# Kernel tuning notes

Hardware: AMD Instinct MI355X
Metric: run time of the kernel (lower is better)

## Reference

```python
import jax, jax.numpy as jnp
import numpy as np

N_NODES = 20000
N_EDGES = 256000
DIM = 128
N_LAYERS = 4


def _bn(x, gamma, beta, eps=1e-5):
    # BatchNorm1d in training mode: batch statistics over the node/edge axis
    mu = x.mean(0)
    var = ((x - mu) ** 2).mean(0)
    return gamma * (x - mu) * jax.lax.rsqrt(var + eps) + beta


def setup_inputs() -> dict:
    key = jax.random.key(0)
    ks = jax.random.split(key, 32)
    s = 1.0 / np.sqrt(DIM)
    inp = {
        'h': jax.random.normal(ks[0], (N_NODES, DIM), jnp.float32),
        'e': jax.random.normal(ks[1], (N_EDGES, DIM), jnp.float32),
        'src': jax.random.randint(ks[2], (N_EDGES,), 0, N_NODES, jnp.int32),
        'dst': jax.random.randint(ks[3], (N_EDGES,), 0, N_NODES, jnp.int32),
        'W_emb_h': jax.random.normal(ks[4], (DIM, DIM), jnp.float32) * s,
        'b_emb_h': jnp.zeros((DIM,), jnp.float32),
        'W_emb_e': jax.random.normal(ks[5], (DIM, DIM), jnp.float32) * s,
        'b_emb_e': jnp.zeros((DIM,), jnp.float32),
    }
    for i, nm in enumerate(['A', 'B', 'C', 'D', 'E']):
        inp[nm + 'w'] = jax.random.normal(ks[6 + i], (N_LAYERS, DIM, DIM), jnp.float32) * s
        inp[nm + 'b'] = jnp.zeros((N_LAYERS, DIM), jnp.float32)
    inp['gh'] = jnp.ones((N_LAYERS, DIM), jnp.float32)
    inp['bh'] = jnp.zeros((N_LAYERS, DIM), jnp.float32)
    inp['ge'] = jnp.ones((N_LAYERS, DIM), jnp.float32)
    inp['be'] = jnp.zeros((N_LAYERS, DIM), jnp.float32)
    return inp


def reference(h, e, src, dst, W_emb_h, b_emb_h, W_emb_e, b_emb_e,
              Aw, Ab, Bw, Bb, Cw, Cb, Dw, Db, Ew, Eb, gh, bh, ge, be):
    n_nodes = h.shape[0]
    # input embeddings
    h = h @ W_emb_h + b_emb_h
    e = e @ W_emb_e + b_emb_e
    for l in range(Aw.shape[0]):
        h_in, e_in = h, e
        Ah = h @ Aw[l] + Ab[l]
        Bh = h @ Bw[l] + Bb[l]
        Dh = h @ Dw[l] + Db[l]
        Eh = h @ Ew[l] + Eb[l]
        Ce = e @ Cw[l] + Cb[l]
        # edge gates: e_ij = D h_i + E h_j + C e_ij  (edge i->j)
        e_new = Dh[src] + Eh[dst] + Ce            # [E, D]
        sigma = jax.nn.sigmoid(e_new)
        num = jax.ops.segment_sum(sigma * Bh[src], dst, num_segments=n_nodes)
        den = jax.ops.segment_sum(sigma, dst, num_segments=n_nodes)
        h_new = Ah + num / (den + 1e-6)
        h_new = _bn(h_new, gh[l], bh[l])
        e_new = _bn(e_new, ge[l], be[l])
        # relu + residual (dropout = 0)
        h = h_in + jax.nn.relu(h_new)
        e = e_in + jax.nn.relu(e_new)
    return h
```

## Files before the change

### kernel.cpp

```cpp
#include <hip/hip_runtime.h>
#include <hip/hip_bf16.h>

typedef __attribute__((ext_vector_type(8))) short short8;
typedef __attribute__((ext_vector_type(4))) float floatx4;
typedef __attribute__((ext_vector_type(4))) unsigned short ushortx4;

__device__ __forceinline__ float bf2f(unsigned short u) {
    union { float f; unsigned int i; } v; v.i = ((unsigned int)u) << 16; return v.f;
}
__device__ __forceinline__ unsigned short f2bf(float f) {
    union { float f; unsigned int i; } v; v.f = f;
    unsigned int r = v.i + 0x7fffu + ((v.i >> 16) & 1u);
    return (unsigned short)(r >> 16);
}

__global__ void deg_count(const int* __restrict__ dst, int* __restrict__ deg, int E) {
    int i = blockIdx.x * 256 + threadIdx.x;
    if (i < E) atomicAdd(&deg[dst[i]], 1);
}

__global__ __launch_bounds__(1024) void scan_rowptr(const int* __restrict__ deg,
                                                    int* __restrict__ rowptr,
                                                    int* __restrict__ cursor, int N) {
    const int CH = 20;
    __shared__ int buf[1024];
    int t = threadIdx.x;
    int base = t * CH;
    int local[CH];
    int tot = 0;
#pragma unroll
    for (int k = 0; k < CH; ++k) {
        int i = base + k;
        int v = (i < N) ? deg[i] : 0;
        local[k] = tot;
        tot += v;
    }
    buf[t] = tot;
    __syncthreads();
    for (int off = 1; off < 1024; off <<= 1) {
        int x = (t >= off) ? buf[t - off] : 0;
        __syncthreads();
        buf[t] += x;
        __syncthreads();
    }
    int excl = buf[t] - tot;
#pragma unroll
    for (int k = 0; k < CH; ++k) {
        int i = base + k;
        if (i < N) { rowptr[i] = excl + local[k]; cursor[i] = excl + local[k]; }
    }
    if (t == 1023) rowptr[N] = buf[1023];
}

__global__ void scatter_edges(const int* __restrict__ src, const int* __restrict__ dst,
                              int* __restrict__ cursor, int* __restrict__ eix,
                              int* __restrict__ sx, int E) {
    int i = blockIdx.x * 256 + threadIdx.x;
    if (i >= E) return;
    int d = dst[i];
    int pos = atomicAdd(&cursor[d], 1);
    eix[pos] = i;
    sx[pos] = src[i];
}

__global__ void transpose_w(const float* __restrict__ Wh,
                            const float* __restrict__ We,
                            const float* __restrict__ Aw,
                            const float* __restrict__ Bw,
                            const float* __restrict__ Cw,
                            const float* __restrict__ Dw,
                            const float* __restrict__ Ew,
                            unsigned short* __restrict__ Wt) {
    int i = blockIdx.x * 256 + threadIdx.x;
    const int total = 22 * 16384;
    if (i >= total) return;
    int slot = i >> 14;
    int r = i & 16383;
    int n = r >> 7;
    int k = r & 127;
    const float* srcp;
    if (slot == 0) srcp = Wh;
    else if (slot == 1) srcp = We;
    else {
        int t = slot - 2;
        int l = t / 5, w = t % 5;
        const float* bases[5] = {Aw, Bw, Cw, Dw, Ew};
        srcp = bases[w] + l * 16384;
    }
    Wt[i] = f2bf(srcp[k * 128 + n]);
}

template <int IN_BF16, int OUT_BF16, int GATHER>
__global__ __launch_bounds__(256) void gemm128(const void* __restrict__ Ain,
                                               const int* __restrict__ ridx,
                                               const unsigned short* __restrict__ Wt,
                                               const float* __restrict__ bias,
                                               void* __restrict__ Cout, int nStrips) {
    const int lane = threadIdx.x & 63;
    const int wv = threadIdx.x >> 6;
    const int m16 = lane & 15;
    const int kg = lane >> 4;

    short8 b[4][8];
#pragma unroll
    for (int ks = 0; ks < 4; ++ks)
#pragma unroll
        for (int nt = 0; nt < 8; ++nt)
            b[ks][nt] = *(const short8*)(Wt + (nt * 16 + m16) * 128 + ks * 32 + kg * 8);

    float bv[8];
#pragma unroll
    for (int nt = 0; nt < 8; ++nt) bv[nt] = bias[nt * 16 + m16];

    const float* Af = (const float*)Ain;
    const unsigned short* Ab16 = (const unsigned short*)Ain;

    int wave = blockIdx.x * 4 + wv;
    int nw = gridDim.x * 4;
    for (int s = wave; s < nStrips; s += nw) {
        int rowA = s * 16 + m16;
        if (GATHER) rowA = ridx[rowA];
        size_t rowBase = (size_t)rowA * 128;
        short8 a[4];
#pragma unroll
        for (int ks = 0; ks < 4; ++ks) {
            int off = ks * 32 + kg * 8;
            if (IN_BF16) {
                a[ks] = *(const short8*)(Ab16 + rowBase + off);
            } else {
                floatx4 f0 = *(const floatx4*)(Af + rowBase + off);
                floatx4 f1 = *(const floatx4*)(Af + rowBase + off + 4);
                short8 t;
                t[0] = (short)f2bf(f0[0]); t[1] = (short)f2bf(f0[1]);
                t[2] = (short)f2bf(f0[2]); t[3] = (short)f2bf(f0[3]);
                t[4] = (short)f2bf(f1[0]); t[5] = (short)f2bf(f1[1]);
                t[6] = (short)f2bf(f1[2]); t[7] = (short)f2bf(f1[3]);
                a[ks] = t;
            }
        }
        floatx4 acc[8];
#pragma unroll
        for (int nt = 0; nt < 8; ++nt) acc[nt] = (floatx4){0.f, 0.f, 0.f, 0.f};
#pragma unroll
        for (int ks = 0; ks < 4; ++ks)
#pragma unroll
            for (int nt = 0; nt < 8; ++nt)
                acc[nt] = __builtin_amdgcn_mfma_f32_16x16x32_bf16(a[ks], b[ks][nt], acc[nt], 0, 0, 0);
#pragma unroll
        for (int nt = 0; nt < 8; ++nt) {
#pragma unroll
            for (int i = 0; i < 4; ++i) {
                size_t r = (size_t)s * 16 + kg * 4 + i;
                int cix = nt * 16 + m16;
                float v = acc[nt][i] + bv[nt];
                if (OUT_BF16)
                    ((unsigned short*)Cout)[r * 128 + cix] = f2bf(v);
                else
                    ((float*)Cout)[r * 128 + cix] = v;
            }
        }
    }
}

__global__ __launch_bounds__(256) void gemm_h4(const float* __restrict__ h_cur,
                                               const unsigned short* __restrict__ WtL,
                                               const float* __restrict__ Abi,
                                               const float* __restrict__ Bbi,
                                               const float* __restrict__ Dbi,
                                               const float* __restrict__ Ebi,
                                               float* __restrict__ AhB,
                                               unsigned short* __restrict__ BD16,
                                               unsigned short* __restrict__ Eh16,
                                               int nStrips) {
    const int lane = threadIdx.x & 63;
    const int wv = threadIdx.x >> 6;
    const int m16 = lane & 15;
    const int kg = lane >> 4;
    int s = blockIdx.x;
    if (s >= nStrips) return;

    const int slotmap[4] = {0, 1, 3, 4};
    const unsigned short* Wm = WtL + slotmap[wv] * 16384;
    const float* biasp = (wv == 0) ? Abi : (wv == 1) ? Bbi : (wv == 2) ? Dbi : Ebi;

    short8 b[4][8];
#pragma unroll
    for (int ks = 0; ks < 4; ++ks)
#pragma unroll
        for (int nt = 0; nt < 8; ++nt)
            b[ks][nt] = *(const short8*)(Wm + (nt * 16 + m16) * 128 + ks * 32 + kg * 8);
    float bv[8];
#pragma unroll
    for (int nt = 0; nt < 8; ++nt) bv[nt] = biasp[nt * 16 + m16];

    size_t rowBase = ((size_t)s * 16 + m16) * 128;
    short8 a[4];
#pragma unroll
    for (int ks = 0; ks < 4; ++ks) {
        int off = ks * 32 + kg * 8;
        floatx4 f0 = *(const floatx4*)(h_cur + rowBase + off);
        floatx4 f1 = *(const floatx4*)(h_cur + rowBase + off + 4);
        short8 t;
        t[0] = (short)f2bf(f0[0]); t[1] = (short)f2bf(f0[1]);
        t[2] = (short)f2bf(f0[2]); t[3] = (short)f2bf(f0[3]);
        t[4] = (short)f2bf(f1[0]); t[5] = (short)f2bf(f1[1]);
        t[6] = (short)f2bf(f1[2]); t[7] = (short)f2bf(f1[3]);
        a[ks] = t;
    }
    floatx4 acc[8];
#pragma unroll
    for (int nt = 0; nt < 8; ++nt) acc[nt] = (floatx4){0.f, 0.f, 0.f, 0.f};
#pragma unroll
    for (int ks = 0; ks < 4; ++ks)
#pragma unroll
        for (int nt = 0; nt < 8; ++nt)
            acc[nt] = __builtin_amdgcn_mfma_f32_16x16x32_bf16(a[ks], b[ks][nt], acc[nt], 0, 0, 0);

#pragma unroll
    for (int nt = 0; nt < 8; ++nt)
#pragma unroll
        for (int i = 0; i < 4; ++i) {
            size_t r = (size_t)s * 16 + kg * 4 + i;
            int c = nt * 16 + m16;
            float v = acc[nt][i] + bv[nt];
            if (wv == 0) AhB[r * 128 + c] = v;
            else if (wv == 1) BD16[r * 256 + 2 * c] = f2bf(v);
            else if (wv == 2) BD16[r * 256 + 2 * c + 1] = f2bf(v);
            else Eh16[r * 128 + c] = f2bf(v);
        }
}

template <int DO_E>
__global__ __launch_bounds__(256) void node_aggregate(unsigned short* __restrict__ Ce,
                                                      const unsigned short* __restrict__ BD16,
                                                      const unsigned short* __restrict__ Eh16,
                                                      const int* __restrict__ rowptr,
                                                      const int* __restrict__ sx,
                                                      const float* __restrict__ Ah,
                                                      float* __restrict__ h_new,
                                                      float* __restrict__ sums, int N) {
    const int q = threadIdx.x & 31;
    const int g = threadIdx.x >> 5;
    float hs[4] = {0.f, 0.f, 0.f, 0.f};
    float hq[4] = {0.f, 0.f, 0.f, 0.f};
    float es[4] = {0.f, 0.f, 0.f, 0.f};
    float eq[4] = {0.f, 0.f, 0.f, 0.f};
    for (int d = blockIdx.x * 8 + g; d < N; d += gridDim.x * 8) {
        int beg = rowptr[d], end = rowptr[d + 1];
        ushortx4 eh4 = *(const ushortx4*)(Eh16 + (size_t)d * 128 + q * 4);
        float ehf[4];
#pragma unroll
        for (int k = 0; k < 4; ++k) ehf[k] = bf2f(eh4[k]);
        float num[4] = {0.f, 0.f, 0.f, 0.f};
        float den[4] = {0.f, 0.f, 0.f, 0.f};
        int j = beg;
        for (; j + 1 < end; j += 2) {
            int s0 = sx[j], s1 = sx[j + 1];
            ushortx4 c0 = *(const ushortx4*)(Ce + (size_t)j * 128 + q * 4);
            ushortx4 c1 = *(const ushortx4*)(Ce + (size_t)(j + 1) * 128 + q * 4);
            short8 bd0 = *(const short8*)(BD16 + (size_t)s0 * 256 + q * 8);
            short8 bd1 = *(const short8*)(BD16 + (size_t)s1 * 256 + q * 8);
            ushortx4 o0, o1;
#pragma unroll
            for (int k = 0; k < 4; ++k) {
                float en0 = bf2f(c0[k]) + bf2f((unsigned short)bd0[2 * k + 1]) + ehf[k];
                float en1 = bf2f(c1[k]) + bf2f((unsigned short)bd1[2 * k + 1]) + ehf[k];
                if (DO_E) {
                    es[k] += en0 + en1;
                    eq[k] += en0 * en0 + en1 * en1;
                    o0[k] = f2bf(en0);
                    o1[k] = f2bf(en1);
                }
                float sg0 = 1.f / (1.f + __expf(-en0));
                float sg1 = 1.f / (1.f + __expf(-en1));
                den[k] += sg0 + sg1;
                num[k] += sg0 * bf2f((unsigned short)bd0[2 * k])
                        + sg1 * bf2f((unsigned short)bd1[2 * k]);
            }
            if (DO_E) {
                *(ushortx4*)(Ce + (size_t)j * 128 + q * 4) = o0;
                *(ushortx4*)(Ce + (size_t)(j + 1) * 128 + q * 4) = o1;
            }
        }
        if (j < end) {
            int s0 = sx[j];
            ushortx4 c0 = *(const ushortx4*)(Ce + (size_t)j * 128 + q * 4);
            short8 bd0 = *(const short8*)(BD16 + (size_t)s0 * 256 + q * 8);
            ushortx4 o0;
#pragma unroll
            for (int k = 0; k < 4; ++k) {
                float en0 = bf2f(c0[k]) + bf2f((unsigned short)bd0[2 * k + 1]) + ehf[k];
                if (DO_E) {
                    es[k] += en0;
                    eq[k] += en0 * en0;
                    o0[k] = f2bf(en0);
                }
                float sg0 = 1.f / (1.f + __expf(-en0));
                den[k] += sg0;
                num[k] += sg0 * bf2f((unsigned short)bd0[2 * k]);
            }
            if (DO_E) *(ushortx4*)(Ce + (size_t)j * 128 + q * 4) = o0;
        }
        floatx4 ah = *(const floatx4*)(Ah + (size_t)d * 128 + q * 4);
        floatx4 out;
#pragma unroll
        for (int k = 0; k < 4; ++k) {
            float v = ah[k] + num[k] / (den[k] + 1e-6f);
            out[k] = v;
            hs[k] += v;
            hq[k] += v * v;
        }
        *(floatx4*)(h_new + (size_t)d * 128 + q * 4) = out;
    }
    __shared__ float ls[512];
    ls[threadIdx.x] = 0.f;
    ls[256 + threadIdx.x] = 0.f;
    __syncthreads();
#pragma unroll
    for (int k = 0; k < 4; ++k) {
        atomicAdd(&ls[q * 4 + k], hs[k]);
        atomicAdd(&ls[128 + q * 4 + k], hq[k]);
        if (DO_E) {
            atomicAdd(&ls[256 + q * 4 + k], es[k]);
            atomicAdd(&ls[384 + q * 4 + k], eq[k]);
        }
    }
    __syncthreads();
    atomicAdd(&sums[threadIdx.x], ls[threadIdx.x]);
    if (DO_E) atomicAdd(&sums[256 + threadIdx.x], ls[256 + threadIdx.x]);
}

__global__ void finalize_stats(const float* __restrict__ sums,
                               const float* __restrict__ gh,
                               const float* __restrict__ bh,
                               const float* __restrict__ ge,
                               const float* __restrict__ be,
                               float* __restrict__ coef, int N, int E) {
    int c = threadIdx.x;
    if (c >= 128) return;
    float muh = sums[c] / (float)N;
    float vh = fmaxf(sums[128 + c] / (float)N - muh * muh, 0.f);
    float rsh = rsqrtf(vh + 1e-5f);
    float g = gh[c], bt = bh[c];
    coef[c] = g * rsh;
    coef[128 + c] = bt - g * rsh * muh;
    float mue = sums[256 + c] / (float)E;
    float ve = fmaxf(sums[384 + c] / (float)E - mue * mue, 0.f);
    float rse = rsqrtf(ve + 1e-5f);
    float g2 = ge[c], b2 = be[c];
    coef[256 + c] = g2 * rse;
    coef[384 + c] = b2 - g2 * rse * mue;
}

__global__ __launch_bounds__(256) void h_update(const float* __restrict__ h_new,
                                                const float* __restrict__ coef,
                                                float* __restrict__ h_cur,
                                                float* __restrict__ out, int N) {
    const int c = threadIdx.x & 127;
    float sa = coef[c], sb = coef[128 + c];
    int total = N * 128;
    for (int i = blockIdx.x * blockDim.x + threadIdx.x; i < total; i += gridDim.x * blockDim.x) {
        float v = h_new[i] * sa + sb;
        v = v > 0.f ? v : 0.f;
        float h = h_cur[i] + v;
        h_cur[i] = h;
        if (out) out[i] = h;
    }
}

__global__ __launch_bounds__(256) void e_update(const unsigned short* __restrict__ e_new,
                                                const float* __restrict__ coef,
                                                unsigned short* __restrict__ e_cur, int E) {
    int total8 = E * 16;
    for (int idx = blockIdx.x * blockDim.x + threadIdx.x; idx < total8;
         idx += gridDim.x * blockDim.x) {
        int c8 = (idx & 15) * 8;
        short8 en = *(const short8*)(e_new + (size_t)idx * 8);
        short8 ec = *(const short8*)(e_cur + (size_t)idx * 8);
        floatx4 sa0 = *(const floatx4*)(coef + 256 + c8);
        floatx4 sa1 = *(const floatx4*)(coef + 256 + c8 + 4);
        floatx4 sb0 = *(const floatx4*)(coef + 384 + c8);
        floatx4 sb1 = *(const floatx4*)(coef + 384 + c8 + 4);
        short8 r;
#pragma unroll
        for (int k = 0; k < 8; ++k) {
            float sa = (k < 4) ? sa0[k] : sa1[k - 4];
            float sb = (k < 4) ? sb0[k] : sb1[k - 4];
            float v = bf2f((unsigned short)en[k]) * sa + sb;
            v = v > 0.f ? v : 0.f;
            r[k] = (short)f2bf(bf2f((unsigned short)ec[k]) + v);
        }
        *(short8*)(e_cur + (size_t)idx * 8) = r;
    }
}

extern "C" void kernel_launch(void* const* d_in, const int* in_sizes, int n_in,
                              void* d_out, int out_size, void* d_ws, size_t ws_size,
                              hipStream_t stream) {
    const int N = 20000, E = 256000, L = 4;

    const float* h_in = (const float*)d_in[0];
    const float* e_in = (const float*)d_in[1];
    const int* src = (const int*)d_in[2];
    const int* dst = (const int*)d_in[3];
    const float* Wemb_h = (const float*)d_in[4];
    const float* bemb_h = (const float*)d_in[5];
    const float* Wemb_e = (const float*)d_in[6];
    const float* bemb_e = (const float*)d_in[7];
    const float* Aw = (const float*)d_in[8];
    const float* Abi = (const float*)d_in[9];
    const float* Bw = (const float*)d_in[10];
    const float* Bbi = (const float*)d_in[11];
    const float* Cw = (const float*)d_in[12];
    const float* Cbi = (const float*)d_in[13];
    const float* Dw = (const float*)d_in[14];
    const float* Dbi = (const float*)d_in[15];
    const float* Ew = (const float*)d_in[16];
    const float* Ebi = (const float*)d_in[17];
    const float* gh = (const float*)d_in[18];
    const float* bh = (const float*)d_in[19];
    const float* ge = (const float*)d_in[20];
    const float* be = (const float*)d_in[21];

    char* p = (char*)d_ws;
    auto carve = [&](size_t bytes) {
        void* r = (void*)p;
        p += ((bytes + 255) & ~(size_t)255);
        return r;
    };
    unsigned short* Wt = (unsigned short*)carve((size_t)22 * 16384 * 2);
    float* h_cur = (float*)carve((size_t)N * 128 * 4);
    unsigned short* e_cur = (unsigned short*)carve((size_t)E * 128 * 2);
    unsigned short* e_new = (unsigned short*)carve((size_t)E * 128 * 2);
    float* AhB = (float*)carve((size_t)N * 128 * 4);
    unsigned short* BD16 = (unsigned short*)carve((size_t)N * 256 * 2);
    unsigned short* Eh16 = (unsigned short*)carve((size_t)N * 128 * 2);
    float* h_newB = (float*)carve((size_t)N * 128 * 4);
    float* sums = (float*)carve(4 * 128 * 4);
    float* coef = (float*)carve(4 * 128 * 4);
    int* deg = (int*)carve((size_t)N * 4);
    int* rowptr = (int*)carve((size_t)(N + 1) * 4);
    int* cursor = (int*)carve((size_t)N * 4);
    int* eix = (int*)carve((size_t)E * 4);
    int* sx = (int*)carve((size_t)E * 4);

    hipMemsetAsync(deg, 0, (size_t)N * 4, stream);
    deg_count<<<(E + 255) / 256, 256, 0, stream>>>(dst, deg, E);
    scan_rowptr<<<1, 1024, 0, stream>>>(deg, rowptr, cursor, N);
    scatter_edges<<<(E + 255) / 256, 256, 0, stream>>>(src, dst, cursor, eix, sx, E);

    transpose_w<<<(22 * 16384 + 255) / 256, 256, 0, stream>>>(Wemb_h, Wemb_e, Aw, Bw, Cw, Dw, Ew, Wt);

    gemm128<0, 0, 0><<<313, 256, 0, stream>>>(h_in, nullptr, Wt + 0 * 16384, bemb_h, h_cur, N / 16);
    gemm128<0, 1, 1><<<2048, 256, 0, stream>>>(e_in, eix, Wt + 1 * 16384, bemb_e, e_cur, E / 16);

    for (int l = 0; l < L; ++l) {
        int last = (l == L - 1);
        hipMemsetAsync(sums, 0, 4 * 128 * 4, stream);
        const unsigned short* WtL = Wt + (size_t)(2 + l * 5) * 16384;
        gemm_h4<<<N / 16, 256, 0, stream>>>(h_cur, WtL, Abi + l * 128, Bbi + l * 128,
                                            Dbi + l * 128, Ebi + l * 128, AhB, BD16, Eh16,
                                            N / 16);
        gemm128<1, 1, 0><<<2048, 256, 0, stream>>>(e_cur, nullptr, WtL + 2 * 16384, Cbi + l * 128,
                                                   e_new, E / 16);
        if (!last)
            node_aggregate<1><<<1250, 256, 0, stream>>>(e_new, BD16, Eh16, rowptr, sx, AhB,
                                                        h_newB, sums, N);
        else
            node_aggregate<0><<<1250, 256, 0, stream>>>(e_new, BD16, Eh16, rowptr, sx, AhB,
                                                        h_newB, sums, N);
        finalize_stats<<<1, 128, 0, stream>>>(sums, gh + l * 128, bh + l * 128, ge + l * 128,
                                              be + l * 128, coef, N, E);
        h_update<<<512, 256, 0, stream>>>(h_newB, coef, h_cur, last ? (float*)d_out : nullptr, N);
        if (!last) e_update<<<2048, 256, 0, stream>>>(e_new, coef, e_cur, E);
    }
}
```

Baseline: 1.117 ms.

## Split GEMM output columns across waves, swap MFMA operands, prefetch next strip

Both GEMM kernels are reorganized so each wave owns only two 16-column output tiles instead of all eight. The four waves of a block now share one 16-row strip rather than each processing its own, which cuts per-wave weight registers from 32 to 8 short8 fragments. MFMA operands are swapped so accumulators hold consecutive columns, allowing vectorized 4-wide stores instead of scalar strided writes. gemm128 also software-prefetches the next strip's A rows, and gemm_h4 becomes a 1024-thread persistent kernel whose 16 waves split the A/E/B/D outputs, with packed BD16 stores; grid sizes are retuned. The trade-off is that each A row is loaded redundantly by all waves of a block and there are fewer MFMAs per load.

```diff
diff --git a/kernel.cpp b/kernel.cpp
--- a/kernel.cpp
+++ b/kernel.cpp
@@ -101,27 +101,29 @@
     const int m16 = lane & 15;
     const int kg = lane >> 4;
 
-    short8 b[4][8];
-#pragma unroll
-    for (int ks = 0; ks < 4; ++ks)
-#pragma unroll
-        for (int nt = 0; nt < 8; ++nt)
-            b[ks][nt] = *(const short8*)(Wt + (nt * 16 + m16) * 128 + ks * 32 + kg * 8);
-
-    float bv[8];
-#pragma unroll
-    for (int nt = 0; nt < 8; ++nt) bv[nt] = bias[nt * 16 + m16];
+    short8 b[4][2];
+#pragma unroll
+    for (int j = 0; j < 2; ++j)
+#pragma unroll
+        for (int ks = 0; ks < 4; ++ks)
+            b[ks][j] = *(const short8*)(Wt + ((wv * 2 + j) * 16 + m16) * 128 + ks * 32 + kg * 8);
+
+    floatx4 bv[2];
+#pragma unroll
+    for (int j = 0; j < 2; ++j)
+        bv[j] = *(const floatx4*)(bias + (wv * 2 + j) * 16 + kg * 4);
 
     const float* Af = (const float*)Ain;
     const unsigned short* Ab16 = (const unsigned short*)Ain;
 
-    int wave = blockIdx.x * 4 + wv;
-    int nw = gridDim.x * 4;
-    for (int s = wave; s < nStrips; s += nw) {
+    const int stride = gridDim.x;
+    int s0 = blockIdx.x;
+    if (s0 >= nStrips) return;
+
+    auto loadA = [&](int s, short8* a) {
         int rowA = s * 16 + m16;
         if (GATHER) rowA = ridx[rowA];
         size_t rowBase = (size_t)rowA * 128;
-        short8 a[4];
 #pragma unroll
         for (int ks = 0; ks < 4; ++ks) {
             int off = ks * 32 + kg * 8;
@@ -138,96 +140,137 @@
                 a[ks] = t;
             }
         }
-        floatx4 acc[8];
-#pragma unroll
-        for (int nt = 0; nt < 8; ++nt) acc[nt] = (floatx4){0.f, 0.f, 0.f, 0.f};
-#pragma unroll
-        for (int ks = 0; ks < 4; ++ks)
-#pragma unroll
-            for (int nt = 0; nt < 8; ++nt)
-                acc[nt] = __builtin_amdgcn_mfma_f32_16x16x32_bf16(a[ks], b[ks][nt], acc[nt], 0, 0, 0);
-#pragma unroll
-        for (int nt = 0; nt < 8; ++nt) {
-#pragma unroll
-            for (int i = 0; i < 4; ++i) {
-                size_t r = (size_t)s * 16 + kg * 4 + i;
-                int cix = nt * 16 + m16;
-                float v = acc[nt][i] + bv[nt];
-                if (OUT_BF16)
-                    ((unsigned short*)Cout)[r * 128 + cix] = f2bf(v);
-                else
-                    ((float*)Cout)[r * 128 + cix] = v;
-            }
-        }
-    }
-}
-
-__global__ __launch_bounds__(256) void gemm_h4(const float* __restrict__ h_cur,
-                                               const unsigned short* __restrict__ WtL,
-                                               const float* __restrict__ Abi,
-                                               const float* __restrict__ Bbi,
-                                               const float* __restrict__ Dbi,
-                                               const float* __restrict__ Ebi,
-                                               float* __restrict__ AhB,
-                                               unsigned short* __restrict__ BD16,
-                                               unsigned short* __restrict__ Eh16,
-                                               int nStrips) {
+    };
+
+    short8 a0[4], a1[4];
+    loadA(s0, a0);
+    for (int s = s0; s < nStrips; s += stride) {
+        int sn = s + stride;
+        if (sn < nStrips) loadA(sn, a1);
+
+        floatx4 acc[2];
+        acc[0] = (floatx4){0.f, 0.f, 0.f, 0.f};
+        acc[1] = (floatx4){0.f, 0.f, 0.f, 0.f};
+#pragma unroll
+        for (int ks = 0; ks < 4; ++ks) {
+            acc[0] = __builtin_amdgcn_mfma_f32_16x16x32_bf16(b[ks][0], a0[ks], acc[0], 0, 0, 0);
+            acc[1] = __builtin_amdgcn_mfma_f32_16x16x32_bf16(b[ks][1], a0[ks], acc[1], 0, 0, 0);
+        }
+
+        size_t rbase = ((size_t)s * 16 + m16) * 128;
+#pragma unroll
+        for (int j = 0; j < 2; ++j) {
+            int c0 = (wv * 2 + j) * 16 + kg * 4;
+            if (OUT_BF16) {
+                ushortx4 o;
+#pragma unroll
+                for (int i = 0; i < 4; ++i) o[i] = f2bf(acc[j][i] + bv[j][i]);
+                *(ushortx4*)((unsigned short*)Cout + rbase + c0) = o;
+            } else {
+                floatx4 o;
+#pragma unroll
+                for (int i = 0; i < 4; ++i) o[i] = acc[j][i] + bv[j][i];
+                *(floatx4*)((float*)Cout + rbase + c0) = o;
+            }
+        }
+#pragma unroll
+        for (int ks = 0; ks < 4; ++ks) a0[ks] = a1[ks];
+    }
+}
+
+__global__ __launch_bounds__(1024) void gemm_h4(const float* __restrict__ h_cur,
+                                                const unsigned short* __restrict__ WtL,
+                                                const float* __restrict__ Abi,
+                                                const float* __restrict__ Bbi,
+                                                const float* __restrict__ Dbi,
+                                                const float* __restrict__ Ebi,
+                                                float* __restrict__ AhB,
+                                                unsigned short* __restrict__ BD16,
+                                                unsigned short* __restrict__ Eh16,
+                                                int nStrips) {
     const int lane = threadIdx.x & 63;
-    const int wv = threadIdx.x >> 6;
+    const int w = threadIdx.x >> 6;
     const int m16 = lane & 15;
     const int kg = lane >> 4;
-    int s = blockIdx.x;
-    if (s >= nStrips) return;
-
-    const int slotmap[4] = {0, 1, 3, 4};
-    const unsigned short* Wm = WtL + slotmap[wv] * 16384;
-    const float* biasp = (wv == 0) ? Abi : (wv == 1) ? Bbi : (wv == 2) ? Dbi : Ebi;
-
-    short8 b[4][8];
-#pragma unroll
-    for (int ks = 0; ks < 4; ++ks)
-#pragma unroll
-        for (int nt = 0; nt < 8; ++nt)
-            b[ks][nt] = *(const short8*)(Wm + (nt * 16 + m16) * 128 + ks * 32 + kg * 8);
-    float bv[8];
-#pragma unroll
-    for (int nt = 0; nt < 8; ++nt) bv[nt] = biasp[nt * 16 + m16];
-
-    size_t rowBase = ((size_t)s * 16 + m16) * 128;
-    short8 a[4];
-#pragma unroll
-    for (int ks = 0; ks < 4; ++ks) {
-        int off = ks * 32 + kg * 8;
-        floatx4 f0 = *(const floatx4*)(h_cur + rowBase + off);
-        floatx4 f1 = *(const floatx4*)(h_cur + rowBase + off + 4);
-        short8 t;
-        t[0] = (short)f2bf(f0[0]); t[1] = (short)f2bf(f0[1]);
-        t[2] = (short)f2bf(f0[2]); t[3] = (short)f2bf(f0[3]);
-        t[4] = (short)f2bf(f1[0]); t[5] = (short)f2bf(f1[1]);
-        t[6] = (short)f2bf(f1[2]); t[7] = (short)f2bf(f1[3]);
-        a[ks] = t;
-    }
-    floatx4 acc[8];
-#pragma unroll
-    for (int nt = 0; nt < 8; ++nt) acc[nt] = (floatx4){0.f, 0.f, 0.f, 0.f};
-#pragma unroll
-    for (int ks = 0; ks < 4; ++ks)
-#pragma unroll
-        for (int nt = 0; nt < 8; ++nt)
-            acc[nt] = __builtin_amdgcn_mfma_f32_16x16x32_bf16(a[ks], b[ks][nt], acc[nt], 0, 0, 0);
-
-#pragma unroll
-    for (int nt = 0; nt < 8; ++nt)
-#pragma unroll
-        for (int i = 0; i < 4; ++i) {
-            size_t r = (size_t)s * 16 + kg * 4 + i;
-            int c = nt * 16 + m16;
-            float v = acc[nt][i] + bv[nt];
-            if (wv == 0) AhB[r * 128 + c] = v;
-            else if (wv == 1) BD16[r * 256 + 2 * c] = f2bf(v);
-            else if (wv == 2) BD16[r * 256 + 2 * c + 1] = f2bf(v);
-            else Eh16[r * 128 + c] = f2bf(v);
-        }
+
+    short8 bf[4][2];
+    floatx4 bv[2];
+    if (w < 8) {
+        const int slot = (w < 4) ? 0 : 4;
+        const float* bp = (w < 4) ? Abi : Ebi;
+        const int ntb = (w & 3) * 2;
+#pragma unroll
+        for (int j = 0; j < 2; ++j) {
+#pragma unroll
+            for (int ks = 0; ks < 4; ++ks)
+                bf[ks][j] = *(const short8*)(WtL + slot * 16384 +
+                                             ((ntb + j) * 16 + m16) * 128 + ks * 32 + kg * 8);
+            bv[j] = *(const floatx4*)(bp + (ntb + j) * 16 + kg * 4);
+        }
+    } else {
+        const int nt = w - 8;
+#pragma unroll
+        for (int ks = 0; ks < 4; ++ks) {
+            bf[ks][0] = *(const short8*)(WtL + 1 * 16384 + (nt * 16 + m16) * 128 + ks * 32 + kg * 8);
+            bf[ks][1] = *(const short8*)(WtL + 3 * 16384 + (nt * 16 + m16) * 128 + ks * 32 + kg * 8);
+        }
+        bv[0] = *(const floatx4*)(Bbi + nt * 16 + kg * 4);
+        bv[1] = *(const floatx4*)(Dbi + nt * 16 + kg * 4);
+    }
+
+    for (int s = blockIdx.x; s < nStrips; s += gridDim.x) {
+        size_t rowBase = ((size_t)s * 16 + m16) * 128;
+        short8 a[4];
+#pragma unroll
+        for (int ks = 0; ks < 4; ++ks) {
+            int off = ks * 32 + kg * 8;
+            floatx4 f0 = *(const floatx4*)(h_cur + rowBase + off);
+            floatx4 f1 = *(const floatx4*)(h_cur + rowBase + off + 4);
+            short8 t;
+            t[0] = (short)f2bf(f0[0]); t[1] = (short)f2bf(f0[1]);
+            t[2] = (short)f2bf(f0[2]); t[3] = (short)f2bf(f0[3]);
+            t[4] = (short)f2bf(f1[0]); t[5] = (short)f2bf(f1[1]);
+            t[6] = (short)f2bf(f1[2]); t[7] = (short)f2bf(f1[3]);
+            a[ks] = t;
+        }
+
+        floatx4 acc0 = (floatx4){0.f, 0.f, 0.f, 0.f};
+        floatx4 acc1 = (floatx4){0.f, 0.f, 0.f, 0.f};
+#pragma unroll
+        for (int ks = 0; ks < 4; ++ks) {
+            acc0 = __builtin_amdgcn_mfma_f32_16x16x32_bf16(bf[ks][0], a[ks], acc0, 0, 0, 0);
+            acc1 = __builtin_amdgcn_mfma_f32_16x16x32_bf16(bf[ks][1], a[ks], acc1, 0, 0, 0);
+        }
+
+        size_t r = (size_t)s * 16 + m16;
+        if (w < 4) {
+            const int ntb = (w & 3) * 2;
+            floatx4 o0, o1;
+#pragma unroll
+            for (int i = 0; i < 4; ++i) { o0[i] = acc0[i] + bv[0][i]; o1[i] = acc1[i] + bv[1][i]; }
+            *(floatx4*)(AhB + r * 128 + (ntb + 0) * 16 + kg * 4) = o0;
+            *(floatx4*)(AhB + r * 128 + (ntb + 1) * 16 + kg * 4) = o1;
+        } else if (w < 8) {
+            const int ntb = (w & 3) * 2;
+            ushortx4 o0, o1;
+#pragma unroll
+            for (int i = 0; i < 4; ++i) {
+                o0[i] = f2bf(acc0[i] + bv[0][i]);
+                o1[i] = f2bf(acc1[i] + bv[1][i]);
+            }
+            *(ushortx4*)(Eh16 + r * 128 + (ntb + 0) * 16 + kg * 4) = o0;
+            *(ushortx4*)(Eh16 + r * 128 + (ntb + 1) * 16 + kg * 4) = o1;
+        } else {
+            const int nt = w - 8;
+            short8 o;
+#pragma unroll
+            for (int i = 0; i < 4; ++i) {
+                o[2 * i]     = (short)f2bf(acc0[i] + bv[0][i]);
+                o[2 * i + 1] = (short)f2bf(acc1[i] + bv[1][i]);
+            }
+            *(short8*)(BD16 + r * 256 + (nt * 16 + kg * 4) * 2) = o;
+        }
+    }
 }
 
 template <int DO_E>
@@ -451,17 +494,17 @@
 
     transpose_w<<<(22 * 16384 + 255) / 256, 256, 0, stream>>>(Wemb_h, Wemb_e, Aw, Bw, Cw, Dw, Ew, Wt);
 
-    gemm128<0, 0, 0><<<313, 256, 0, stream>>>(h_in, nullptr, Wt + 0 * 16384, bemb_h, h_cur, N / 16);
-    gemm128<0, 1, 1><<<2048, 256, 0, stream>>>(e_in, eix, Wt + 1 * 16384, bemb_e, e_cur, E / 16);
+    gemm128<0, 0, 0><<<1024, 256, 0, stream>>>(h_in, nullptr, Wt + 0 * 16384, bemb_h, h_cur, N / 16);
+    gemm128<0, 1, 1><<<1024, 256, 0, stream>>>(e_in, eix, Wt + 1 * 16384, bemb_e, e_cur, E / 16);
 
     for (int l = 0; l < L; ++l) {
         int last = (l == L - 1);
         hipMemsetAsync(sums, 0, 4 * 128 * 4, stream);
         const unsigned short* WtL = Wt + (size_t)(2 + l * 5) * 16384;
-        gemm_h4<<<N / 16, 256, 0, stream>>>(h_cur, WtL, Abi + l * 128, Bbi + l * 128,
-                                            Dbi + l * 128, Ebi + l * 128, AhB, BD16, Eh16,
-                                            N / 16);
-        gemm128<1, 1, 0><<<2048, 256, 0, stream>>>(e_cur, nullptr, WtL + 2 * 16384, Cbi + l * 128,
+        gemm_h4<<<250, 1024, 0, stream>>>(h_cur, WtL, Abi + l * 128, Bbi + l * 128,
+                                          Dbi + l * 128, Ebi + l * 128, AhB, BD16, Eh16,
+                                          N / 16);
+        gemm128<1, 1, 0><<<1024, 256, 0, stream>>>(e_cur, nullptr, WtL + 2 * 16384, Cbi + l * 128,
                                                    e_new, E / 16);
         if (!last)
             node_aggregate<1><<<1250, 256, 0, stream>>>(e_new, BD16, Eh16, rowptr, sx, AhB,
```

New measurement: 1.061 ms. 1.05x faster.
